# Optimization experiments

Hardware: AMD Instinct MI355X
Metric: run time of the kernel (lower is better)

## Reference

```python
import jax, jax.numpy as jnp
import numpy as np

B, D, H, G = 32768, 768, 256, 8
GS = D // G          # group size = 96
MIN_G, MAX_G = 2, 6  # min/max active groups


def setup_inputs() -> dict:
    key = jax.random.key(0)
    ks = jax.random.split(key, 12)
    s = 0.02
    return {
        "query_embedding": jax.random.normal(ks[0], (B, D), jnp.float32),
        # router_net: Linear(D,H) -> LayerNorm(H) -> GELU -> Linear(H,H//2) -> GELU -> Linear(H//2,G)
        "w1": jax.random.normal(ks[1], (D, H), jnp.float32) * s,
        "b1": jnp.zeros((H,), jnp.float32),
        "ln_g": jnp.ones((H,), jnp.float32),
        "ln_b": jnp.zeros((H,), jnp.float32),
        "w2": jax.random.normal(ks[2], (H, H // 2), jnp.float32) * s,
        "b2": jnp.zeros((H // 2,), jnp.float32),
        "w3": jax.random.normal(ks[3], (H // 2, G), jnp.float32) * s,
        "b3": jnp.zeros((G,), jnp.float32),
        # dim_importance: Linear(D,H) -> GELU -> Linear(H,D) (bias init 2.0) -> Sigmoid
        "dw1": jax.random.normal(ks[4], (D, H), jnp.float32) * s,
        "db1": jnp.zeros((H,), jnp.float32),
        "dw2": jax.random.normal(ks[5], (H, D), jnp.float32) * s,
        "db2": jnp.full((D,), 2.0, jnp.float32),
        "group_importance": jax.random.normal(ks[6], (G,), jnp.float32) * s,
    }


def _gelu(x):
    return jax.nn.gelu(x, approximate=False)  # torch nn.GELU default = exact erf


def _layernorm(x, g, b, eps=1e-5):
    mu = jnp.mean(x, axis=-1, keepdims=True)
    var = jnp.var(x, axis=-1, keepdims=True)
    return (x - mu) * jax.lax.rsqrt(var + eps) * g + b


def reference(query_embedding, w1, b1, ln_g, ln_b, w2, b2, w3, b3,
              dw1, db1, dw2, db2, group_importance):
    x = query_embedding
    # router_net (eval mode: dropout is identity, sigmoid gating not gumbel)
    h1 = _gelu(_layernorm(x @ w1 + b1, ln_g, ln_b))
    h2 = _gelu(h1 @ w2 + b2)
    group_logits = h2 @ w3 + b3 + group_importance          # [B, G]
    group_probs = jax.nn.sigmoid(group_logits)

    # constrained hard selection: top MIN_G always on; ranks MIN_G..MAX_G-1 on iff prob > 0.5
    order = jnp.argsort(-group_probs, axis=-1)              # descending sort indices [B, G]
    sorted_probs = jnp.take_along_axis(group_probs, order, axis=-1)
    ranks = jnp.arange(G)
    act_sorted = jnp.where(ranks < MIN_G, 1.0,
                           jnp.where(ranks < MAX_G,
                                     (sorted_probs > 0.5).astype(jnp.float32), 0.0))
    b_idx = jnp.arange(x.shape[0])[:, None]
    hard_mask = jnp.zeros_like(group_probs).at[b_idx, order].set(act_sorted)
    # straight-through estimator
    group_selection = hard_mask - jax.lax.stop_gradient(group_probs) + group_probs

    # expand each group decision over its group_size dims -> [B, D]
    group_mask = jnp.repeat(group_selection, GS, axis=-1)

    dim_weights = jax.nn.sigmoid(_gelu(x @ dw1 + db1) @ dw2 + db2)  # [B, D]
    mask = group_mask * dim_weights

    active_groups = jnp.mean(jnp.sum((group_probs > 0.5).astype(jnp.float32), axis=-1))
    group_usage = jnp.mean((group_probs > 0.5).astype(jnp.float32), axis=0)
    f = jnp.mean(group_probs, axis=0)
    load_balance = G * jnp.sum(f * (1.0 / G))
    active_dims = jnp.mean(jnp.sum((mask > 0.5).astype(jnp.float32), axis=-1))

    return (mask, group_mask, dim_weights, group_probs, group_selection,
            active_groups, group_usage, load_balance, active_dims)
```

## Files before the change

kernel.cpp:

```cpp
#include <hip/hip_runtime.h>
#include <math.h>

#define NB 32768
#define ND 768
#define NH 256
#define NG 8
#define GSZ 96

typedef __attribute__((ext_vector_type(8))) short short8_t;
typedef __attribute__((ext_vector_type(4))) float f32x4;

__device__ __forceinline__ float gelu_exact(float v) {
    return 0.5f * v * (1.0f + erff(v * 0.7071067811865475f));
}
__device__ __forceinline__ float sigmoidf_(float v) {
    return 1.0f / (1.0f + expf(-v));
}
__device__ __forceinline__ unsigned short f2bf(float f) {
    union { float f; unsigned u; } a; a.f = f;
    unsigned r = a.u + 0x7FFF + ((a.u >> 16) & 1);
    return (unsigned short)(r >> 16);
}
__device__ __forceinline__ void f2bf2(float f, unsigned short& hi, unsigned short& lo) {
    union { float f; unsigned u; } a; a.f = f;
    unsigned r = a.u + 0x7FFF + ((a.u >> 16) & 1);
    hi = (unsigned short)(r >> 16);
    union { unsigned u; float f; } hf; hf.u = (r >> 16) << 16;
    float rem = f - hf.f;
    union { float f; unsigned u; } b; b.f = rem;
    unsigned r2 = b.u + 0x7FFF + ((b.u >> 16) & 1);
    lo = (unsigned short)(r2 >> 16);
}

__global__ __launch_bounds__(256) void cvt_wall(
    const float* __restrict__ w1, const float* __restrict__ dw1,
    const float* __restrict__ dw2, unsigned short* __restrict__ w1Th,
    unsigned short* __restrict__ w1Tl, unsigned short* __restrict__ dw1T,
    unsigned short* __restrict__ dw2T)
{
    const int b = blockIdx.x, t = threadIdx.x;
    if (b < 96) {
        int idx = b * 256 + t;
        int k8 = idx >> 8, c = idx & 255;
        short8_t h, lo;
        #pragma unroll
        for (int j = 0; j < 8; ++j) {
            unsigned short hi_, lo_;
            f2bf2(w1[(size_t)(k8 * 8 + j) * 256 + c], hi_, lo_);
            h[j] = (short)hi_; lo[j] = (short)lo_;
        }
        *(short8_t*)(w1Th + (size_t)c * 768 + k8 * 8) = h;
        *(short8_t*)(w1Tl + (size_t)c * 768 + k8 * 8) = lo;
    } else if (b < 192) {
        int idx = (b - 96) * 256 + t;
        int k8 = idx >> 8, c = idx & 255;
        short8_t h;
        #pragma unroll
        for (int j = 0; j < 8; ++j)
            h[j] = (short)f2bf(dw1[(size_t)(k8 * 8 + j) * 256 + c]);
        *(short8_t*)(dw1T + (size_t)c * 768 + k8 * 8) = h;
    } else {
        int idx = (b - 192) * 256 + t;
        int k8 = idx / 768, c = idx - k8 * 768;
        short8_t h;
        #pragma unroll
        for (int j = 0; j < 8; ++j)
            h[j] = (short)f2bf(dw2[(size_t)(k8 * 8 + j) * 768 + c]);
        *(short8_t*)(dw2T + (size_t)c * 256 + k8 * 8) = h;
    }
}

__global__ __launch_bounds__(256) void mfma_u1(
    const float* __restrict__ x, const unsigned short* __restrict__ BTh,
    const unsigned short* __restrict__ BTl, float* __restrict__ u1)
{
    __shared__ unsigned short Ah[128][40];
    __shared__ unsigned short Al[128][40];
    __shared__ unsigned short Bh[128][40];
    __shared__ unsigned short Bl[128][40];

    const int tid = threadIdx.x;
    const int l = tid & 63;
    const int w = tid >> 6;
    const int wm = w >> 1, wn = w & 1;
    const int lg = l >> 4, lr = l & 15;
    const int rb = blockIdx.x >> 1;
    const int cb = blockIdx.x & 1;
    const int rowsBase = rb * 128, colBase = cb * 128;

    f32x4 acc[4][4];
    #pragma unroll
    for (int mi = 0; mi < 4; ++mi)
        #pragma unroll
        for (int ni = 0; ni < 4; ++ni) acc[mi][ni] = (f32x4){0.f, 0.f, 0.f, 0.f};

    for (int kb = 0; kb < ND; kb += 32) {
        #pragma unroll
        for (int m = 0; m < 2; ++m) {
            int flat = m * 256 + tid;
            int row = flat >> 2, seg = flat & 3;
            const float* src = x + (size_t)(rowsBase + row) * ND + kb + seg * 8;
            float4 v0 = *(const float4*)src;
            float4 v1 = *(const float4*)(src + 4);
            float f[8] = {v0.x, v0.y, v0.z, v0.w, v1.x, v1.y, v1.z, v1.w};
            short8_t ph, pl;
            #pragma unroll
            for (int j = 0; j < 8; ++j) {
                unsigned short hi_, lo_;
                f2bf2(f[j], hi_, lo_);
                ph[j] = (short)hi_; pl[j] = (short)lo_;
            }
            *(short8_t*)&Ah[row][seg * 8] = ph;
            *(short8_t*)&Al[row][seg * 8] = pl;
        }
        #pragma unroll
        for (int m = 0; m < 2; ++m) {
            int flat = m * 256 + tid;
            int col = flat >> 2, seg = flat & 3;
            size_t off = (size_t)(colBase + col) * ND + kb + seg * 8;
            *(short8_t*)&Bh[col][seg * 8] = *(const short8_t*)(BTh + off);
            *(short8_t*)&Bl[col][seg * 8] = *(const short8_t*)(BTl + off);
        }
        __syncthreads();

        short8_t afh[4], afl[4], bfh[4], bfl[4];
        #pragma unroll
        for (int mi = 0; mi < 4; ++mi) {
            afh[mi] = *(const short8_t*)&Ah[wm * 64 + mi * 16 + lr][lg * 8];
            afl[mi] = *(const short8_t*)&Al[wm * 64 + mi * 16 + lr][lg * 8];
        }
        #pragma unroll
        for (int ni = 0; ni < 4; ++ni) {
            bfh[ni] = *(const short8_t*)&Bh[wn * 64 + ni * 16 + lr][lg * 8];
            bfl[ni] = *(const short8_t*)&Bl[wn * 64 + ni * 16 + lr][lg * 8];
        }
        #pragma unroll
        for (int mi = 0; mi < 4; ++mi)
            #pragma unroll
            for (int ni = 0; ni < 4; ++ni) {
                acc[mi][ni] = __builtin_amdgcn_mfma_f32_16x16x32_bf16(
                    afl[mi], bfh[ni], acc[mi][ni], 0, 0, 0);
                acc[mi][ni] = __builtin_amdgcn_mfma_f32_16x16x32_bf16(
                    afh[mi], bfl[ni], acc[mi][ni], 0, 0, 0);
                acc[mi][ni] = __builtin_amdgcn_mfma_f32_16x16x32_bf16(
                    afh[mi], bfh[ni], acc[mi][ni], 0, 0, 0);
            }
        __syncthreads();
    }

    #pragma unroll
    for (int ni = 0; ni < 4; ++ni) {
        int col = colBase + wn * 64 + ni * 16 + lr;
        #pragma unroll
        for (int mi = 0; mi < 4; ++mi) {
            int rbase = rowsBase + wm * 64 + mi * 16 + lg * 4;
            #pragma unroll
            for (int j = 0; j < 4; ++j)
                u1[(size_t)(rbase + j) * 256 + col] = acc[mi][ni][j];
        }
    }
}

template<int ACT, int AF32>
__global__ __launch_bounds__(256) void mfma_hi(
    const void* __restrict__ Ap, const unsigned short* __restrict__ BT,
    const float* __restrict__ bias, void* __restrict__ outp,
    int N, int K, int colBlocks)
{
    __shared__ unsigned short As[128][40];
    __shared__ unsigned short Bs[128][40];

    const int tid = threadIdx.x;
    const int l = tid & 63;
    const int w = tid >> 6;
    const int wm = w >> 1, wn = w & 1;
    const int lg = l >> 4, lr = l & 15;
    const int rb = blockIdx.x / colBlocks;
    const int cb = blockIdx.x - rb * colBlocks;
    const int rowsBase = rb * 128, colBase = cb * 128;

    f32x4 acc[4][4];
    #pragma unroll
    for (int mi = 0; mi < 4; ++mi)
        #pragma unroll
        for (int ni = 0; ni < 4; ++ni) acc[mi][ni] = (f32x4){0.f, 0.f, 0.f, 0.f};

    for (int kb = 0; kb < K; kb += 32) {
        if (AF32) {
            const float* A = (const float*)Ap;
            #pragma unroll
            for (int m = 0; m < 2; ++m) {
                int flat = m * 256 + tid;
                int row = flat >> 2, seg = flat & 3;
                const float* src = A + (size_t)(rowsBase + row) * K + kb + seg * 8;
                float4 v0 = *(const float4*)src;
                float4 v1 = *(const float4*)(src + 4);
                float f[8] = {v0.x, v0.y, v0.z, v0.w, v1.x, v1.y, v1.z, v1.w};
                short8_t h;
                #pragma unroll
                for (int j = 0; j < 8; ++j) h[j] = (short)f2bf(f[j]);
                *(short8_t*)&As[row][seg * 8] = h;
            }
        } else {
            const unsigned short* A = (const unsigned short*)Ap;
            #pragma unroll
            for (int m = 0; m < 2; ++m) {
                int flat = m * 256 + tid;
                int row = flat >> 2, seg = flat & 3;
                *(short8_t*)&As[row][seg * 8] =
                    *(const short8_t*)(A + (size_t)(rowsBase + row) * K + kb + seg * 8);
            }
        }
        #pragma unroll
        for (int m = 0; m < 2; ++m) {
            int flat = m * 256 + tid;
            int col = flat >> 2, seg = flat & 3;
            *(short8_t*)&Bs[col][seg * 8] =
                *(const short8_t*)(BT + (size_t)(colBase + col) * K + kb + seg * 8);
        }
        __syncthreads();

        short8_t af[4], bf[4];
        #pragma unroll
        for (int mi = 0; mi < 4; ++mi)
            af[mi] = *(const short8_t*)&As[wm * 64 + mi * 16 + lr][lg * 8];
        #pragma unroll
        for (int ni = 0; ni < 4; ++ni)
            bf[ni] = *(const short8_t*)&Bs[wn * 64 + ni * 16 + lr][lg * 8];
        #pragma unroll
        for (int mi = 0; mi < 4; ++mi)
            #pragma unroll
            for (int ni = 0; ni < 4; ++ni)
                acc[mi][ni] = __builtin_amdgcn_mfma_f32_16x16x32_bf16(
                    af[mi], bf[ni], acc[mi][ni], 0, 0, 0);
        __syncthreads();
    }

    #pragma unroll
    for (int ni = 0; ni < 4; ++ni) {
        int col = colBase + wn * 64 + ni * 16 + lr;
        float bv = bias[col];
        #pragma unroll
        for (int mi = 0; mi < 4; ++mi) {
            int rbase = rowsBase + wm * 64 + mi * 16 + lg * 4;
            #pragma unroll
            for (int j = 0; j < 4; ++j) {
                float v = acc[mi][ni][j] + bv;
                if (ACT == 0) {
                    ((unsigned short*)outp)[(size_t)(rbase + j) * N + col] =
                        f2bf(gelu_exact(v));
                } else {
                    ((float*)outp)[(size_t)(rbase + j) * N + col] = sigmoidf_(v);
                }
            }
        }
    }
}

__global__ __launch_bounds__(256) void k1_epi(
    const float* __restrict__ u1, const float* __restrict__ b1,
    const float* __restrict__ lng, const float* __restrict__ lnb,
    float* __restrict__ h1)
{
    const int wv = threadIdx.x >> 6, l = threadIdx.x & 63;
    const int row = blockIdx.x * 4 + wv;
    float4 a = *(const float4*)(u1 + (size_t)row * 256 + l * 4);
    float4 bb = *(const float4*)(b1 + l * 4);
    float u[4] = {a.x + bb.x, a.y + bb.y, a.z + bb.z, a.w + bb.w};
    float s = u[0] + u[1] + u[2] + u[3];
    float q = u[0]*u[0] + u[1]*u[1] + u[2]*u[2] + u[3]*u[3];
    #pragma unroll
    for (int o = 1; o < 64; o <<= 1) {
        s += __shfl_xor(s, o);
        q += __shfl_xor(q, o);
    }
    float mean = s * (1.0f / 256.0f);
    float var  = q * (1.0f / 256.0f) - mean * mean;
    float rstd = rsqrtf(var + 1e-5f);
    float4 g = *(const float4*)(lng + l * 4);
    float4 be = *(const float4*)(lnb + l * 4);
    float4 o;
    o.x = gelu_exact((u[0] - mean) * rstd * g.x + be.x);
    o.y = gelu_exact((u[1] - mean) * rstd * g.y + be.y);
    o.z = gelu_exact((u[2] - mean) * rstd * g.z + be.z);
    o.w = gelu_exact((u[3] - mean) * rstd * g.w + be.w);
    *(float4*)(h1 + (size_t)row * 256 + l * 4) = o;
}

__global__ __launch_bounds__(256) void k2a_p(
    const float* __restrict__ h1, const float* __restrict__ w2,
    float* __restrict__ u2p)
{
    __shared__ float xs[32][132];
    __shared__ float ws[32][128];

    const int tid = threadIdx.x;
    const int tc = tid & 15, tr = tid >> 4;
    const int c0 = tc * 4, c1 = 64 + tc * 4, r0 = tr * 8;
    const int rb = blockIdx.x >> 1, half = blockIdx.x & 1;
    const int rowsBase = rb * 128, kBase = half * 128;

    float acc[8][8];
    #pragma unroll
    for (int i = 0; i < 8; ++i)
        #pragma unroll
        for (int j = 0; j < 8; ++j) acc[i][j] = 0.0f;

    for (int kc = 0; kc < 4; ++kc) {
        const int kb = kBase + kc * 32;
        #pragma unroll
        for (int m = 0; m < 4; ++m) {
            int flat = m * 256 + tid;
            int r = flat >> 3, i4 = flat & 7;
            float4 v = *(const float4*)(h1 + (size_t)(rowsBase + r) * 256 + kb + i4 * 4);
            xs[i4*4+0][r] = v.x; xs[i4*4+1][r] = v.y;
            xs[i4*4+2][r] = v.z; xs[i4*4+3][r] = v.w;
        }
        #pragma unroll
        for (int m = 0; m < 4; ++m) {
            int flat = m * 256 + tid;
            int k = flat >> 5, c = (flat & 31) * 4;
            *(float4*)&ws[k][c] = *(const float4*)(w2 + (size_t)(kb + k) * 128 + c);
        }
        __syncthreads();
        #pragma unroll 8
        for (int k = 0; k < 32; ++k) {
            float xv[8], wv8[8];
            *(float4*)&xv[0]  = *(const float4*)&xs[k][r0];
            *(float4*)&xv[4]  = *(const float4*)&xs[k][r0 + 4];
            *(float4*)&wv8[0] = *(const float4*)&ws[k][c0];
            *(float4*)&wv8[4] = *(const float4*)&ws[k][c1];
            #pragma unroll
            for (int i = 0; i < 8; ++i)
                #pragma unroll
                for (int j = 0; j < 8; ++j)
                    acc[i][j] = fmaf(xv[i], wv8[j], acc[i][j]);
        }
        __syncthreads();
    }
    float* dst = u2p + (size_t)half * 4194304;
    #pragma unroll
    for (int i = 0; i < 8; ++i) {
        int row = rowsBase + r0 + i;
        *(float4*)(dst + (size_t)row * 128 + c0) = *(float4*)&acc[i][0];
        *(float4*)(dst + (size_t)row * 128 + c1) = *(float4*)&acc[i][4];
    }
}

__global__ __launch_bounds__(128) void k3_router(
    const float* __restrict__ u2p, const float* __restrict__ w3,
    const float* __restrict__ b3, const float* __restrict__ gi,
    const float* __restrict__ b2, float* __restrict__ probsOut,
    float* __restrict__ selOut, float* __restrict__ scal)
{
    __shared__ float ws3[128][8];
    __shared__ float sAct[2], sP[2], sCnt[2][8];

    const int tid = threadIdx.x;
    *(float4*)&ws3[tid][0] = *(const float4*)(w3 + tid * 8);
    *(float4*)&ws3[tid][4] = *(const float4*)(w3 + tid * 8 + 4);
    __syncthreads();

    const int row = blockIdx.x * 128 + tid;
    const float* r0p = u2p + (size_t)row * 128;
    const float* r1p = u2p + 4194304 + (size_t)row * 128;

    float accg[8];
    #pragma unroll
    for (int g = 0; g < 8; ++g) accg[g] = 0.0f;
    #pragma unroll 4
    for (int k4 = 0; k4 < 32; ++k4) {
        float4 a = *(const float4*)(r0p + k4 * 4);
        float4 b = *(const float4*)(r1p + k4 * 4);
        float4 bb = *(const float4*)(b2 + k4 * 4);
        float hv4[4];
        hv4[0] = gelu_exact(a.x + b.x + bb.x);
        hv4[1] = gelu_exact(a.y + b.y + bb.y);
        hv4[2] = gelu_exact(a.z + b.z + bb.z);
        hv4[3] = gelu_exact(a.w + b.w + bb.w);
        #pragma unroll
        for (int t = 0; t < 4; ++t)
            #pragma unroll
            for (int g = 0; g < 8; ++g)
                accg[g] = fmaf(hv4[t], ws3[k4 * 4 + t][g], accg[g]);
    }

    float p[8], gs[8], cnt[8];
    float actCnt = 0.0f, pSum = 0.0f;
    #pragma unroll
    for (int g = 0; g < 8; ++g) {
        float lg = accg[g] + b3[g] + gi[g];
        p[g] = sigmoidf_(lg);
    }
    #pragma unroll
    for (int g = 0; g < 8; ++g) {
        int rank = 0;
        #pragma unroll
        for (int j = 0; j < 8; ++j) {
            rank += (p[j] > p[g]) ? 1 : 0;
            rank += (j < g && p[j] == p[g]) ? 1 : 0;
        }
        float act = (rank < 2) ? 1.0f
                  : ((rank < 6) ? ((p[g] > 0.5f) ? 1.0f : 0.0f) : 0.0f);
        gs[g] = (act - p[g]) + p[g];
        float over = (p[g] > 0.5f) ? 1.0f : 0.0f;
        cnt[g] = over;
        actCnt += over;
        pSum += p[g];
    }

    *(float4*)(probsOut + (size_t)row * 8)     = *(float4*)&p[0];
    *(float4*)(probsOut + (size_t)row * 8 + 4) = *(float4*)&p[4];
    *(float4*)(selOut   + (size_t)row * 8)     = *(float4*)&gs[0];
    *(float4*)(selOut   + (size_t)row * 8 + 4) = *(float4*)&gs[4];

    #pragma unroll
    for (int o = 32; o > 0; o >>= 1) {
        actCnt += __shfl_down(actCnt, o);
        pSum   += __shfl_down(pSum, o);
        #pragma unroll
        for (int g = 0; g < 8; ++g) cnt[g] += __shfl_down(cnt[g], o);
    }
    if ((tid & 63) == 0) {
        int w = tid >> 6;
        sAct[w] = actCnt; sP[w] = pSum;
        #pragma unroll
        for (int g = 0; g < 8; ++g) sCnt[w][g] = cnt[g];
    }
    __syncthreads();
    if (tid == 0) {
        const float invB = 1.0f / 32768.0f;
        atomicAdd(&scal[0], (sAct[0] + sAct[1]) * invB);
        atomicAdd(&scal[9], (sP[0] + sP[1]) * invB);
        #pragma unroll
        for (int g = 0; g < 8; ++g)
            atomicAdd(&scal[1 + g], (sCnt[0][g] + sCnt[1][g]) * invB);
    }
}

__global__ __launch_bounds__(256) void k4_mask(
    const float* __restrict__ sel, const float* __restrict__ dwts,
    float* __restrict__ gmaskOut, float* __restrict__ maskOut,
    float* __restrict__ activeDims)
{
    const int stride = gridDim.x * 256;
    float cntF = 0.0f;
    for (int i4 = blockIdx.x * 256 + threadIdx.x; i4 < 6291456; i4 += stride) {
        int row = i4 / 192;
        int rem = i4 - row * 192;
        int g = rem / 24;
        float v = sel[(size_t)row * 8 + g];
        float4 d = *(const float4*)(dwts + (size_t)i4 * 4);
        float4 gm = {v, v, v, v};
        float4 m = {v * d.x, v * d.y, v * d.z, v * d.w};
        *(float4*)(gmaskOut + (size_t)i4 * 4) = gm;
        *(float4*)(maskOut  + (size_t)i4 * 4) = m;
        cntF += (m.x > 0.5f ? 1.0f : 0.0f) + (m.y > 0.5f ? 1.0f : 0.0f)
              + (m.z > 0.5f ? 1.0f : 0.0f) + (m.w > 0.5f ? 1.0f : 0.0f);
    }
    #pragma unroll
    for (int o = 32; o > 0; o >>= 1) cntF += __shfl_down(cntF, o);
    __shared__ float sc[4];
    if ((threadIdx.x & 63) == 0) sc[threadIdx.x >> 6] = cntF;
    __syncthreads();
    if (threadIdx.x == 0)
        atomicAdd(activeDims, (sc[0] + sc[1] + sc[2] + sc[3]) * (1.0f / 32768.0f));
}

__global__ void kz_zero(float* s) { if (threadIdx.x < 11) s[threadIdx.x] = 0.0f; }

extern "C" void kernel_launch(void* const* d_in, const int* in_sizes, int n_in,
                              void* d_out, int out_size, void* d_ws, size_t ws_size,
                              hipStream_t stream)
{
    const float* x   = (const float*)d_in[0];
    const float* w1  = (const float*)d_in[1];
    const float* b1  = (const float*)d_in[2];
    const float* lng = (const float*)d_in[3];
    const float* lnb = (const float*)d_in[4];
    const float* w2  = (const float*)d_in[5];
    const float* b2  = (const float*)d_in[6];
    const float* w3  = (const float*)d_in[7];
    const float* b3  = (const float*)d_in[8];
    const float* dw1 = (const float*)d_in[9];
    const float* db1 = (const float*)d_in[10];
    const float* dw2 = (const float*)d_in[11];
    const float* db2 = (const float*)d_in[12];
    const float* gi  = (const float*)d_in[13];

    float* out   = (float*)d_out;
    float* mask  = out;
    float* gmask = out + 25165824;
    float* dwts  = out + 50331648;
    float* probs = out + 75497472;
    float* sel   = out + 75759616;
    float* scal  = out + 76021760;

    float* u1  = mask;
    float* h1  = mask + 8388608;
    float* u2p = mask + 16777216;
    unsigned short* g1h  = (unsigned short*)gmask;
    unsigned short* w1Th = (unsigned short*)(gmask + 4194304);
    unsigned short* w1Tl = (unsigned short*)(gmask + 4292608);
    unsigned short* dw1T = (unsigned short*)(gmask + 4390912);
    unsigned short* dw2T = (unsigned short*)(gmask + 4489216);

    kz_zero<<<dim3(1), dim3(64), 0, stream>>>(scal);
    cvt_wall<<<dim3(288), dim3(256), 0, stream>>>(
        w1, dw1, dw2, w1Th, w1Tl, dw1T, dw2T);
    mfma_u1<<<dim3(512), dim3(256), 0, stream>>>(x, w1Th, w1Tl, u1);
    k1_epi<<<dim3(8192), dim3(256), 0, stream>>>(u1, b1, lng, lnb, h1);
    k2a_p<<<dim3(512), dim3(256), 0, stream>>>(h1, w2, u2p);
    k3_router<<<dim3(256), dim3(128), 0, stream>>>(
        u2p, w3, b3, gi, b2, probs, sel, scal);
    mfma_hi<0, 1><<<dim3(512), dim3(256), 0, stream>>>(
        (const void*)x, dw1T, db1, (void*)g1h, 256, 768, 2);
    mfma_hi<1, 0><<<dim3(1536), dim3(256), 0, stream>>>(
        (const void*)g1h, dw2T, db2, (void*)dwts, 768, 256, 6);
    k4_mask<<<dim3(2048), dim3(256), 0, stream>>>(sel, dwts, gmask, mask, &scal[10]);
}
```

Before: 308.0 us.

## Fuse LayerNorm+GELU into first router GEMM and use split-bf16 MFMA for second

The first router GEMM now gives each block 64 rows with all 256 columns, so the LayerNorm statistics and GELU can be computed in its epilogue. That removes the separate u1 write/read and the k1_epi launch. The second router GEMM replaces the scalar FP32 split-K kernel with a 3-pass split-bf16 MFMA kernel on pre-transposed w2, which drops the partial-sum buffer and its extra read in the router kernel. In exchange the fused kernel stages a full 256-column B tile per block, so it uses more LDS and has lower occupancy.

```diff
diff --git a/kernel.cpp b/kernel.cpp
--- a/kernel.cpp
+++ b/kernel.cpp
@@ -34,9 +34,10 @@
 
 __global__ __launch_bounds__(256) void cvt_wall(
     const float* __restrict__ w1, const float* __restrict__ dw1,
-    const float* __restrict__ dw2, unsigned short* __restrict__ w1Th,
-    unsigned short* __restrict__ w1Tl, unsigned short* __restrict__ dw1T,
-    unsigned short* __restrict__ dw2T)
+    const float* __restrict__ dw2, const float* __restrict__ w2,
+    unsigned short* __restrict__ w1Th, unsigned short* __restrict__ w1Tl,
+    unsigned short* __restrict__ dw1T, unsigned short* __restrict__ dw2T,
+    unsigned short* __restrict__ w2Th, unsigned short* __restrict__ w2Tl)
 {
     const int b = blockIdx.x, t = threadIdx.x;
     if (b < 96) {
@@ -59,7 +60,7 @@
         for (int j = 0; j < 8; ++j)
             h[j] = (short)f2bf(dw1[(size_t)(k8 * 8 + j) * 256 + c]);
         *(short8_t*)(dw1T + (size_t)c * 768 + k8 * 8) = h;
-    } else {
+    } else if (b < 288) {
         int idx = (b - 192) * 256 + t;
         int k8 = idx / 768, c = idx - k8 * 768;
         short8_t h;
@@ -67,12 +68,171 @@
         for (int j = 0; j < 8; ++j)
             h[j] = (short)f2bf(dw2[(size_t)(k8 * 8 + j) * 768 + c]);
         *(short8_t*)(dw2T + (size_t)c * 256 + k8 * 8) = h;
-    }
-}
-
-__global__ __launch_bounds__(256) void mfma_u1(
+    } else {
+        int idx = (b - 288) * 256 + t;
+        int k8 = idx >> 7, c = idx & 127;
+        short8_t h, lo;
+        #pragma unroll
+        for (int j = 0; j < 8; ++j) {
+            unsigned short hi_, lo_;
+            f2bf2(w2[(size_t)(k8 * 8 + j) * 128 + c], hi_, lo_);
+            h[j] = (short)hi_; lo[j] = (short)lo_;
+        }
+        *(short8_t*)(w2Th + (size_t)c * 256 + k8 * 8) = h;
+        *(short8_t*)(w2Tl + (size_t)c * 256 + k8 * 8) = lo;
+    }
+}
+
+__global__ __launch_bounds__(256) void mfma_h1(
     const float* __restrict__ x, const unsigned short* __restrict__ BTh,
-    const unsigned short* __restrict__ BTl, float* __restrict__ u1)
+    const unsigned short* __restrict__ BTl, const float* __restrict__ b1,
+    const float* __restrict__ lng, const float* __restrict__ lnb,
+    float* __restrict__ h1)
+{
+    __shared__ unsigned short Ah[64][40];
+    __shared__ unsigned short Al[64][40];
+    __shared__ unsigned short Bh[256][40];
+    __shared__ unsigned short Bl[256][40];
+    __shared__ float sS[4][64];
+    __shared__ float sQ[4][64];
+
+    const int tid = threadIdx.x;
+    const int l = tid & 63;
+    const int wn = tid >> 6;
+    const int lg = l >> 4, lr = l & 15;
+    const int rowsBase = blockIdx.x * 64;
+
+    f32x4 acc[4][4];
+    #pragma unroll
+    for (int mi = 0; mi < 4; ++mi)
+        #pragma unroll
+        for (int ni = 0; ni < 4; ++ni) acc[mi][ni] = (f32x4){0.f, 0.f, 0.f, 0.f};
+
+    for (int kb = 0; kb < ND; kb += 32) {
+        {
+            int row = tid >> 2, seg = tid & 3;
+            const float* src = x + (size_t)(rowsBase + row) * ND + kb + seg * 8;
+            float4 v0 = *(const float4*)src;
+            float4 v1 = *(const float4*)(src + 4);
+            float f[8] = {v0.x, v0.y, v0.z, v0.w, v1.x, v1.y, v1.z, v1.w};
+            short8_t ph, pl;
+            #pragma unroll
+            for (int j = 0; j < 8; ++j) {
+                unsigned short hi_, lo_;
+                f2bf2(f[j], hi_, lo_);
+                ph[j] = (short)hi_; pl[j] = (short)lo_;
+            }
+            *(short8_t*)&Ah[row][seg * 8] = ph;
+            *(short8_t*)&Al[row][seg * 8] = pl;
+        }
+        #pragma unroll
+        for (int m = 0; m < 4; ++m) {
+            int flat = m * 256 + tid;
+            int col = flat >> 2, seg = flat & 3;
+            size_t off = (size_t)col * ND + kb + seg * 8;
+            *(short8_t*)&Bh[col][seg * 8] = *(const short8_t*)(BTh + off);
+            *(short8_t*)&Bl[col][seg * 8] = *(const short8_t*)(BTl + off);
+        }
+        __syncthreads();
+
+        short8_t afh[4], afl[4], bfh[4], bfl[4];
+        #pragma unroll
+        for (int mi = 0; mi < 4; ++mi) {
+            afh[mi] = *(const short8_t*)&Ah[mi * 16 + lr][lg * 8];
+            afl[mi] = *(const short8_t*)&Al[mi * 16 + lr][lg * 8];
+        }
+        #pragma unroll
+        for (int ni = 0; ni < 4; ++ni) {
+            bfh[ni] = *(const short8_t*)&Bh[wn * 64 + ni * 16 + lr][lg * 8];
+            bfl[ni] = *(const short8_t*)&Bl[wn * 64 + ni * 16 + lr][lg * 8];
+        }
+        #pragma unroll
+        for (int mi = 0; mi < 4; ++mi)
+            #pragma unroll
+            for (int ni = 0; ni < 4; ++ni) {
+                acc[mi][ni] = __builtin_amdgcn_mfma_f32_16x16x32_bf16(
+                    afl[mi], bfh[ni], acc[mi][ni], 0, 0, 0);
+                acc[mi][ni] = __builtin_amdgcn_mfma_f32_16x16x32_bf16(
+                    afh[mi], bfl[ni], acc[mi][ni], 0, 0, 0);
+                acc[mi][ni] = __builtin_amdgcn_mfma_f32_16x16x32_bf16(
+                    afh[mi], bfh[ni], acc[mi][ni], 0, 0, 0);
+            }
+        __syncthreads();
+    }
+
+    float bv[4];
+    #pragma unroll
+    for (int ni = 0; ni < 4; ++ni) bv[ni] = b1[wn * 64 + ni * 16 + lr];
+
+    float s[4][4], q[4][4];
+    #pragma unroll
+    for (int mi = 0; mi < 4; ++mi)
+        #pragma unroll
+        for (int j = 0; j < 4; ++j) {
+            float ss = 0.f, qq = 0.f;
+            #pragma unroll
+            for (int ni = 0; ni < 4; ++ni) {
+                float u = acc[mi][ni][j] + bv[ni];
+                ss += u; qq += u * u;
+            }
+            s[mi][j] = ss; q[mi][j] = qq;
+        }
+    #pragma unroll
+    for (int o = 1; o < 16; o <<= 1) {
+        #pragma unroll
+        for (int mi = 0; mi < 4; ++mi)
+            #pragma unroll
+            for (int j = 0; j < 4; ++j) {
+                s[mi][j] += __shfl_xor(s[mi][j], o);
+                q[mi][j] += __shfl_xor(q[mi][j], o);
+            }
+    }
+    if (lr == 0) {
+        #pragma unroll
+        for (int mi = 0; mi < 4; ++mi)
+            #pragma unroll
+            for (int j = 0; j < 4; ++j) {
+                int rl = mi * 16 + lg * 4 + j;
+                sS[wn][rl] = s[mi][j];
+                sQ[wn][rl] = q[mi][j];
+            }
+    }
+    __syncthreads();
+
+    float mean[4][4], rstd[4][4];
+    #pragma unroll
+    for (int mi = 0; mi < 4; ++mi)
+        #pragma unroll
+        for (int j = 0; j < 4; ++j) {
+            int rl = mi * 16 + lg * 4 + j;
+            float ss = sS[0][rl] + sS[1][rl] + sS[2][rl] + sS[3][rl];
+            float qq = sQ[0][rl] + sQ[1][rl] + sQ[2][rl] + sQ[3][rl];
+            float m_ = ss * (1.0f / 256.0f);
+            float v_ = qq * (1.0f / 256.0f) - m_ * m_;
+            mean[mi][j] = m_;
+            rstd[mi][j] = rsqrtf(v_ + 1e-5f);
+        }
+
+    #pragma unroll
+    for (int ni = 0; ni < 4; ++ni) {
+        int col = wn * 64 + ni * 16 + lr;
+        float g = lng[col], be = lnb[col];
+        #pragma unroll
+        for (int mi = 0; mi < 4; ++mi) {
+            #pragma unroll
+            for (int j = 0; j < 4; ++j) {
+                int row = rowsBase + mi * 16 + lg * 4 + j;
+                float u = acc[mi][ni][j] + bv[ni];
+                float v = gelu_exact((u - mean[mi][j]) * rstd[mi][j] * g + be);
+                h1[(size_t)row * 256 + col] = v;
+            }
+        }
+    }
+}
+
+__global__ __launch_bounds__(256) void mfma_u2(
+    const float* __restrict__ h1, const unsigned short* __restrict__ BTh,
+    const unsigned short* __restrict__ BTl, float* __restrict__ u2)
 {
     __shared__ unsigned short Ah[128][40];
     __shared__ unsigned short Al[128][40];
@@ -84,9 +244,7 @@
     const int w = tid >> 6;
     const int wm = w >> 1, wn = w & 1;
     const int lg = l >> 4, lr = l & 15;
-    const int rb = blockIdx.x >> 1;
-    const int cb = blockIdx.x & 1;
-    const int rowsBase = rb * 128, colBase = cb * 128;
+    const int rowsBase = blockIdx.x * 128;
 
     f32x4 acc[4][4];
     #pragma unroll
@@ -94,12 +252,12 @@
         #pragma unroll
         for (int ni = 0; ni < 4; ++ni) acc[mi][ni] = (f32x4){0.f, 0.f, 0.f, 0.f};
 
-    for (int kb = 0; kb < ND; kb += 32) {
+    for (int kb = 0; kb < 256; kb += 32) {
         #pragma unroll
         for (int m = 0; m < 2; ++m) {
             int flat = m * 256 + tid;
             int row = flat >> 2, seg = flat & 3;
-            const float* src = x + (size_t)(rowsBase + row) * ND + kb + seg * 8;
+            const float* src = h1 + (size_t)(rowsBase + row) * 256 + kb + seg * 8;
             float4 v0 = *(const float4*)src;
             float4 v1 = *(const float4*)(src + 4);
             float f[8] = {v0.x, v0.y, v0.z, v0.w, v1.x, v1.y, v1.z, v1.w};
@@ -117,7 +275,7 @@
         for (int m = 0; m < 2; ++m) {
             int flat = m * 256 + tid;
             int col = flat >> 2, seg = flat & 3;
-            size_t off = (size_t)(colBase + col) * ND + kb + seg * 8;
+            size_t off = (size_t)col * 256 + kb + seg * 8;
             *(short8_t*)&Bh[col][seg * 8] = *(const short8_t*)(BTh + off);
             *(short8_t*)&Bl[col][seg * 8] = *(const short8_t*)(BTl + off);
         }
@@ -150,13 +308,13 @@
 
     #pragma unroll
     for (int ni = 0; ni < 4; ++ni) {
-        int col = colBase + wn * 64 + ni * 16 + lr;
+        int col = wn * 64 + ni * 16 + lr;
         #pragma unroll
         for (int mi = 0; mi < 4; ++mi) {
             int rbase = rowsBase + wm * 64 + mi * 16 + lg * 4;
             #pragma unroll
             for (int j = 0; j < 4; ++j)
-                u1[(size_t)(rbase + j) * 256 + col] = acc[mi][ni][j];
+                u2[(size_t)(rbase + j) * 128 + col] = acc[mi][ni][j];
         }
     }
 }
@@ -257,98 +415,8 @@
     }
 }
 
-__global__ __launch_bounds__(256) void k1_epi(
-    const float* __restrict__ u1, const float* __restrict__ b1,
-    const float* __restrict__ lng, const float* __restrict__ lnb,
-    float* __restrict__ h1)
-{
-    const int wv = threadIdx.x >> 6, l = threadIdx.x & 63;
-    const int row = blockIdx.x * 4 + wv;
-    float4 a = *(const float4*)(u1 + (size_t)row * 256 + l * 4);
-    float4 bb = *(const float4*)(b1 + l * 4);
-    float u[4] = {a.x + bb.x, a.y + bb.y, a.z + bb.z, a.w + bb.w};
-    float s = u[0] + u[1] + u[2] + u[3];
-    float q = u[0]*u[0] + u[1]*u[1] + u[2]*u[2] + u[3]*u[3];
-    #pragma unroll
-    for (int o = 1; o < 64; o <<= 1) {
-        s += __shfl_xor(s, o);
-        q += __shfl_xor(q, o);
-    }
-    float mean = s * (1.0f / 256.0f);
-    float var  = q * (1.0f / 256.0f) - mean * mean;
-    float rstd = rsqrtf(var + 1e-5f);
-    float4 g = *(const float4*)(lng + l * 4);
-    float4 be = *(const float4*)(lnb + l * 4);
-    float4 o;
-    o.x = gelu_exact((u[0] - mean) * rstd * g.x + be.x);
-    o.y = gelu_exact((u[1] - mean) * rstd * g.y + be.y);
-    o.z = gelu_exact((u[2] - mean) * rstd * g.z + be.z);
-    o.w = gelu_exact((u[3] - mean) * rstd * g.w + be.w);
-    *(float4*)(h1 + (size_t)row * 256 + l * 4) = o;
-}
-
-__global__ __launch_bounds__(256) void k2a_p(
-    const float* __restrict__ h1, const float* __restrict__ w2,
-    float* __restrict__ u2p)
-{
-    __shared__ float xs[32][132];
-    __shared__ float ws[32][128];
-
-    const int tid = threadIdx.x;
-    const int tc = tid & 15, tr = tid >> 4;
-    const int c0 = tc * 4, c1 = 64 + tc * 4, r0 = tr * 8;
-    const int rb = blockIdx.x >> 1, half = blockIdx.x & 1;
-    const int rowsBase = rb * 128, kBase = half * 128;
-
-    float acc[8][8];
-    #pragma unroll
-    for (int i = 0; i < 8; ++i)
-        #pragma unroll
-        for (int j = 0; j < 8; ++j) acc[i][j] = 0.0f;
-
-    for (int kc = 0; kc < 4; ++kc) {
-        const int kb = kBase + kc * 32;
-        #pragma unroll
-        for (int m = 0; m < 4; ++m) {
-            int flat = m * 256 + tid;
-            int r = flat >> 3, i4 = flat & 7;
-            float4 v = *(const float4*)(h1 + (size_t)(rowsBase + r) * 256 + kb + i4 * 4);
-            xs[i4*4+0][r] = v.x; xs[i4*4+1][r] = v.y;
-            xs[i4*4+2][r] = v.z; xs[i4*4+3][r] = v.w;
-        }
-        #pragma unroll
-        for (int m = 0; m < 4; ++m) {
-            int flat = m * 256 + tid;
-            int k = flat >> 5, c = (flat & 31) * 4;
-            *(float4*)&ws[k][c] = *(const float4*)(w2 + (size_t)(kb + k) * 128 + c);
-        }
-        __syncthreads();
-        #pragma unroll 8
-        for (int k = 0; k < 32; ++k) {
-            float xv[8], wv8[8];
-            *(float4*)&xv[0]  = *(const float4*)&xs[k][r0];
-            *(float4*)&xv[4]  = *(const float4*)&xs[k][r0 + 4];
-            *(float4*)&wv8[0] = *(const float4*)&ws[k][c0];
-            *(float4*)&wv8[4] = *(const float4*)&ws[k][c1];
-            #pragma unroll
-            for (int i = 0; i < 8; ++i)
-                #pragma unroll
-                for (int j = 0; j < 8; ++j)
-                    acc[i][j] = fmaf(xv[i], wv8[j], acc[i][j]);
-        }
-        __syncthreads();
-    }
-    float* dst = u2p + (size_t)half * 4194304;
-    #pragma unroll
-    for (int i = 0; i < 8; ++i) {
-        int row = rowsBase + r0 + i;
-        *(float4*)(dst + (size_t)row * 128 + c0) = *(float4*)&acc[i][0];
-        *(float4*)(dst + (size_t)row * 128 + c1) = *(float4*)&acc[i][4];
-    }
-}
-
 __global__ __launch_bounds__(128) void k3_router(
-    const float* __restrict__ u2p, const float* __restrict__ w3,
+    const float* __restrict__ u2, const float* __restrict__ w3,
     const float* __restrict__ b3, const float* __restrict__ gi,
     const float* __restrict__ b2, float* __restrict__ probsOut,
     float* __restrict__ selOut, float* __restrict__ scal)
@@ -362,8 +430,7 @@
     __syncthreads();
 
     const int row = blockIdx.x * 128 + tid;
-    const float* r0p = u2p + (size_t)row * 128;
-    const float* r1p = u2p + 4194304 + (size_t)row * 128;
+    const float* r0p = u2 + (size_t)row * 128;
 
     float accg[8];
     #pragma unroll
@@ -371,13 +438,12 @@
     #pragma unroll 4
     for (int k4 = 0; k4 < 32; ++k4) {
         float4 a = *(const float4*)(r0p + k4 * 4);
-        float4 b = *(const float4*)(r1p + k4 * 4);
         float4 bb = *(const float4*)(b2 + k4 * 4);
         float hv4[4];
-        hv4[0] = gelu_exact(a.x + b.x + bb.x);
-        hv4[1] = gelu_exact(a.y + b.y + bb.y);
-        hv4[2] = gelu_exact(a.z + b.z + bb.z);
-        hv4[3] = gelu_exact(a.w + b.w + bb.w);
+        hv4[0] = gelu_exact(a.x + bb.x);
+        hv4[1] = gelu_exact(a.y + bb.y);
+        hv4[2] = gelu_exact(a.z + bb.z);
+        hv4[3] = gelu_exact(a.w + bb.w);
         #pragma unroll
         for (int t = 0; t < 4; ++t)
             #pragma unroll
@@ -496,23 +562,24 @@
     float* sel   = out + 75759616;
     float* scal  = out + 76021760;
 
-    float* u1  = mask;
-    float* h1  = mask + 8388608;
-    float* u2p = mask + 16777216;
+    float* h1 = mask;
+    float* u2 = mask + 8388608;
     unsigned short* g1h  = (unsigned short*)gmask;
     unsigned short* w1Th = (unsigned short*)(gmask + 4194304);
     unsigned short* w1Tl = (unsigned short*)(gmask + 4292608);
     unsigned short* dw1T = (unsigned short*)(gmask + 4390912);
     unsigned short* dw2T = (unsigned short*)(gmask + 4489216);
+    unsigned short* w2Th = (unsigned short*)(gmask + 4587520);
+    unsigned short* w2Tl = (unsigned short*)(gmask + 4603904);
 
     kz_zero<<<dim3(1), dim3(64), 0, stream>>>(scal);
-    cvt_wall<<<dim3(288), dim3(256), 0, stream>>>(
-        w1, dw1, dw2, w1Th, w1Tl, dw1T, dw2T);
-    mfma_u1<<<dim3(512), dim3(256), 0, stream>>>(x, w1Th, w1Tl, u1);
-    k1_epi<<<dim3(8192), dim3(256), 0, stream>>>(u1, b1, lng, lnb, h1);
-    k2a_p<<<dim3(512), dim3(256), 0, stream>>>(h1, w2, u2p);
+    cvt_wall<<<dim3(304), dim3(256), 0, stream>>>(
+        w1, dw1, dw2, w2, w1Th, w1Tl, dw1T, dw2T, w2Th, w2Tl);
+    mfma_h1<<<dim3(512), dim3(256), 0, stream>>>(
+        x, w1Th, w1Tl, b1, lng, lnb, h1);
+    mfma_u2<<<dim3(256), dim3(256), 0, stream>>>(h1, w2Th, w2Tl, u2);
     k3_router<<<dim3(256), dim3(128), 0, stream>>>(
-        u2p, w3, b3, gi, b2, probs, sel, scal);
+        u2, w3, b3, gi, b2, probs, sel, scal);
     mfma_hi<0, 1><<<dim3(512), dim3(256), 0, stream>>>(
         (const void*)x, dw1T, db1, (void*)g1h, 256, 768, 2);
     mfma_hi<1, 0><<<dim3(1536), dim3(256), 0, stream>>>(
```

Result: slower. 338.3 us (+9.8%).
